# Kernel optimization log

Measured on AMD Instinct MI355X. Metric: run time of the kernel, lower is better.

## Reference

```python
import jax, jax.numpy as jnp
import numpy as np

K = 128
HEADS = 8
B = 4
T = 2048


def setup_inputs() -> dict:
    key = jax.random.key(0)
    ks = jax.random.split(key, 6)
    x = jax.random.normal(ks[0], (B, T, K), dtype=jnp.float32)
    s = 1.0 / np.sqrt(K)
    # torch nn.Linear weights are (out_features, in_features)
    Wq = jax.random.uniform(ks[1], (HEADS * K, K), dtype=jnp.float32, minval=-s, maxval=s)
    Wk = jax.random.uniform(ks[2], (HEADS * K, K), dtype=jnp.float32, minval=-s, maxval=s)
    Wv = jax.random.uniform(ks[3], (HEADS * K, K), dtype=jnp.float32, minval=-s, maxval=s)
    su = 1.0 / np.sqrt(HEADS * K)
    Wu = jax.random.uniform(ks[4], (K, HEADS * K), dtype=jnp.float32, minval=-su, maxval=su)
    bu = jax.random.uniform(ks[5], (K,), dtype=jnp.float32, minval=-su, maxval=su)
    return {"x": x, "Wq": Wq, "Wk": Wk, "Wv": Wv, "Wu": Wu, "bu": bu}


def reference(x, Wq, Wk, Wv, Wu, bu):
    b, t, k = x.shape
    h = HEADS
    # project: Linear(k, k*h) then view(b,t,h,k); weight reshaped to (h, k_out, k_in)
    q = jnp.einsum('btk,hdk->bhtd', x, Wq.reshape(h, k, k))
    kk = jnp.einsum('btk,hdk->bhtd', x, Wk.reshape(h, k, k))
    v = jnp.einsum('btk,hdk->bhtd', x, Wv.reshape(h, k, k))
    scale = jnp.asarray(k, x.dtype) ** 0.25
    q = q / scale
    kk = kk / scale
    dot = jnp.einsum('bhtd,bhsd->bhts', q, kk)  # [b,h,t,t]
    att = jax.nn.softmax(dot, axis=-1)
    out = jnp.einsum('bhts,bhsd->bhtd', att, v)  # [b,h,t,k]
    out = out.transpose(0, 2, 1, 3).reshape(b, t, h * k)
    return out @ Wu.T + bu
```

## Files before the change

### kernel.cpp

```cpp
#include <hip/hip_runtime.h>
#include <cmath>

namespace {

constexpr int HEADS = 8;
constexpr int Bn = 4;
constexpr int Tn = 2048;
constexpr int Dn = 128;
constexpr float Q_PRESCALE = 0.1275174340f;

typedef _Float16 half8 __attribute__((ext_vector_type(8)));
typedef _Float16 half4 __attribute__((ext_vector_type(4)));
typedef _Float16 half2v __attribute__((ext_vector_type(2)));
typedef float f32x4 __attribute__((ext_vector_type(4)));
typedef float f32x16 __attribute__((ext_vector_type(16)));
typedef unsigned int u32;
typedef unsigned int u32x4 __attribute__((ext_vector_type(4)));

__global__ __launch_bounds__(256) void cast_kernel(
    const float* __restrict__ x, const float* __restrict__ Wq, const float* __restrict__ Wk,
    const float* __restrict__ Wv, const float* __restrict__ Wu, _Float16* __restrict__ xh,
    _Float16* __restrict__ WH) {
  const int idx = blockIdx.x * 256 + threadIdx.x;
  const size_t base = (size_t)idx * 8;
  const float* src;
  _Float16* dst;
  if (base < 1048576) {
    src = x + base;
    dst = xh + base;
  } else {
    const size_t r = base - 1048576;
    const int s = (int)(r >> 17);
    src = ((s == 0) ? Wq : (s == 1) ? Wk : (s == 2) ? Wv : Wu) + (r & 131071);
    dst = WH + r;
  }
  const float4 a = *reinterpret_cast<const float4*>(src);
  const float4 b = *reinterpret_cast<const float4*>(src + 4);
  half8 h;
  h[0] = (_Float16)a.x; h[1] = (_Float16)a.y; h[2] = (_Float16)a.z; h[3] = (_Float16)a.w;
  h[4] = (_Float16)b.x; h[5] = (_Float16)b.y; h[6] = (_Float16)b.z; h[7] = (_Float16)b.w;
  *reinterpret_cast<half8*>(dst) = h;
}

__global__ __launch_bounds__(256, 4) void proj_kernel(const _Float16* __restrict__ xh,
                                                      const _Float16* __restrict__ WH,
                                                      _Float16* __restrict__ Qh,
                                                      _Float16* __restrict__ Kh,
                                                      _Float16* __restrict__ Vt) {
  __shared__ _Float16 sB[128 * 136];
  const int tid = threadIdx.x;
  const int w = tid >> 6, lane = tid & 63, quad = lane >> 4, l16 = lane & 15;
  const int m0 = blockIdx.x * 128;
  const int n0 = blockIdx.y * 128;

#pragma unroll
  for (int it = 0; it < 8; ++it) {
    const int fid = tid + it * 256;
    const int r = fid >> 4, g = fid & 15;
    const half8 v = *reinterpret_cast<const half8*>(WH + (size_t)(n0 + r) * 128 + g * 8);
    const int p = g ^ (r & 15);
    *reinterpret_cast<half8*>(sB + r * 128 + p * 8) = v;
  }

  half8 af[2][4];
  const _Float16* xp = xh + (size_t)(m0 + w * 32 + l16) * 128 + quad * 8;
#pragma unroll
  for (int mt = 0; mt < 2; ++mt)
#pragma unroll
    for (int kk = 0; kk < 4; ++kk)
      af[mt][kk] = *reinterpret_cast<const half8*>(xp + mt * 16 * 128 + kk * 32);

  __syncthreads();

  f32x4 acc[2][8];
#pragma unroll
  for (int mt = 0; mt < 2; ++mt)
#pragma unroll
    for (int nt = 0; nt < 8; ++nt) acc[mt][nt] = (f32x4){0.f, 0.f, 0.f, 0.f};

#pragma unroll
  for (int kk = 0; kk < 4; ++kk)
#pragma unroll
    for (int nt = 0; nt < 8; ++nt) {
      const int r = nt * 16 + l16;
      const int p = (kk * 4 + quad) ^ l16;
      const half8 bf = *reinterpret_cast<const half8*>(sB + r * 128 + p * 8);
      acc[0][nt] = __builtin_amdgcn_mfma_f32_16x16x32_f16(af[0][kk], bf, acc[0][nt], 0, 0, 0);
      acc[1][nt] = __builtin_amdgcn_mfma_f32_16x16x32_f16(af[1][kk], bf, acc[1][nt], 0, 0, 0);
    }

  const int sel = n0 >> 10;
  const int h = (n0 >> 7) & 7;
  const int b = m0 >> 11;
  const int t0b = m0 & 2047;
  const int bh = b * HEADS + h;
  const float scale = (sel == 0) ? Q_PRESCALE : 1.0f;

  __syncthreads();

  if (sel < 2) {
#pragma unroll
    for (int mt = 0; mt < 2; ++mt)
#pragma unroll
      for (int nt = 0; nt < 8; ++nt)
#pragma unroll
        for (int r = 0; r < 4; ++r)
          sB[(w * 32 + mt * 16 + quad * 4 + r) * 136 + nt * 16 + l16] =
              (_Float16)(acc[mt][nt][r] * scale);
  } else {
#pragma unroll
    for (int mt = 0; mt < 2; ++mt)
#pragma unroll
      for (int nt = 0; nt < 8; ++nt)
#pragma unroll
        for (int r = 0; r < 4; ++r)
          sB[(nt * 16 + l16) * 136 + w * 32 + mt * 16 + quad * 4 + r] = (_Float16)acc[mt][nt][r];
  }
  __syncthreads();

  _Float16* dstbase;
  size_t rstride;
  if (sel == 0) {
    dstbase = Qh + ((size_t)bh * Tn + t0b) * Dn;
    rstride = Dn;
  } else if (sel == 1) {
    dstbase = Kh + ((size_t)bh * Tn + t0b) * Dn;
    rstride = Dn;
  } else {
    dstbase = Vt + ((size_t)bh * Dn) * Tn + t0b;
    rstride = Tn;
  }
#pragma unroll
  for (int it = 0; it < 8; ++it) {
    const int fid = tid + it * 256;
    const int r = fid >> 4, g = fid & 15;
    const half8 v = *reinterpret_cast<const half8*>(sB + r * 136 + g * 8);
    *reinterpret_cast<half8*>(dstbase + (size_t)r * rstride + g * 8) = v;
  }
}

__global__ __launch_bounds__(512, 2) void flash_kernel(const _Float16* __restrict__ Qh,
                                                       const _Float16* __restrict__ Kh,
                                                       const _Float16* __restrict__ Vt,
                                                       _Float16* __restrict__ Obh) {
  __shared__ _Float16 sAll[40960];

  const int tid = threadIdx.x;
  const int w = tid >> 6;
  const int lane = tid & 63;
  const int l31 = lane & 31;
  const int h = lane >> 5;
  const int lid = blockIdx.x + 8 * blockIdx.y;
  const int xcd = lid & 7, j = lid >> 3;
  const int bh = xcd * 4 + (j >> 3);
  const int qt = j & 7;
  constexpr int NT = Tn / 64;

  half8 qf[8];
  {
    const _Float16* Qp = Qh + ((size_t)bh * Tn + qt * 256 + w * 32 + l31) * Dn + h * 8;
#pragma unroll
    for (int ds = 0; ds < 8; ++ds) qf[ds] = *reinterpret_cast<const half8*>(Qp + ds * 16);
  }

  const _Float16* Kp = Kh + (size_t)bh * Tn * Dn;
  const _Float16* Vp = Vt + (size_t)bh * Dn * Tn;

  f32x16 o[4];
#pragma unroll
  for (int db = 0; db < 4; ++db) o[db] = (f32x16)(0.f);
  float lsum = 0.f;

  half8 kreg[2], vreg[2];
  const int kr = tid >> 4, kg = tid & 15;
  const int vr = tid >> 3, vg = tid & 7;
  const int vG = (vg >> 1) * 2;
  const int vO = (vg & 1) * 4;

#pragma unroll
  for (int it = 0; it < 2; ++it) {
    kreg[it] = *reinterpret_cast<const half8*>(Kp + (size_t)(kr + it * 32) * Dn + kg * 8);
    vreg[it] = *reinterpret_cast<const half8*>(Vp + (size_t)(vr + it * 64) * Tn + vg * 8);
  }
  {
    _Float16* sK0 = sAll;
    _Float16* sV0 = sAll + 16384;
#pragma unroll
    for (int it = 0; it < 2; ++it) {
      const int r = kr + it * 32;
      const int p = kg ^ (r & 15);
      *reinterpret_cast<half8*>(sK0 + r * 128 + p * 8) = kreg[it];
      const int rv = vr + it * 64;
      const int sw = (rv & 7) ^ ((rv >> 1) & 4);
      const half8 v = vreg[it];
      half4 lo, hi;
      lo[0] = v[0]; lo[1] = v[1]; lo[2] = v[2]; lo[3] = v[3];
      hi[0] = v[4]; hi[1] = v[5]; hi[2] = v[6]; hi[3] = v[7];
      *reinterpret_cast<half4*>(sV0 + rv * 64 + ((vG ^ sw) * 8) + vO) = lo;
      *reinterpret_cast<half4*>(sV0 + rv * 64 + (((vG + 1) ^ sw) * 8) + vO) = hi;
    }
  }
#pragma unroll
  for (int it = 0; it < 2; ++it) {
    kreg[it] = *reinterpret_cast<const half8*>(Kp + (size_t)(64 + kr + it * 32) * Dn + kg * 8);
    vreg[it] = *reinterpret_cast<const half8*>(Vp + (size_t)(vr + it * 64) * Tn + 64 + vg * 8);
  }
  __syncthreads();

  f32x16 scA[2], scB[2];
  scA[0] = (f32x16)(0.f);
  scA[1] = (f32x16)(0.f);
#pragma unroll
  for (int ds = 0; ds < 8; ++ds) {
    const int p = (ds * 2 + h) ^ (l31 & 15);
    const half8 kf0 = *reinterpret_cast<const half8*>(sAll + l31 * 128 + p * 8);
    const half8 kf1 = *reinterpret_cast<const half8*>(sAll + (32 + l31) * 128 + p * 8);
    scA[0] = __builtin_amdgcn_mfma_f32_32x32x16_f16(kf0, qf[ds], scA[0], 0, 0, 0);
    scA[1] = __builtin_amdgcn_mfma_f32_32x32x16_f16(kf1, qf[ds], scA[1], 0, 0, 0);
  }

  auto step = [&](int t, f32x16 (&sc)[2], f32x16 (&sn)[2]) {
    _Float16* sKn = sAll + ((t + 1) & 1) * 8192;
    _Float16* sVc = sAll + 16384 + (t % 3) * 8192;
    _Float16* sVn = sAll + 16384 + ((t + 1) % 3) * 8192;

    if (t + 1 < NT) {
#pragma unroll
      for (int it = 0; it < 2; ++it) {
        const int r = kr + it * 32;
        const int p = kg ^ (r & 15);
        *reinterpret_cast<half8*>(sKn + r * 128 + p * 8) = kreg[it];
        const int rv = vr + it * 64;
        const int sw = (rv & 7) ^ ((rv >> 1) & 4);
        const half8 v = vreg[it];
        half4 lo, hi;
        lo[0] = v[0]; lo[1] = v[1]; lo[2] = v[2]; lo[3] = v[3];
        hi[0] = v[4]; hi[1] = v[5]; hi[2] = v[6]; hi[3] = v[7];
        *reinterpret_cast<half4*>(sVn + rv * 64 + ((vG ^ sw) * 8) + vO) = lo;
        *reinterpret_cast<half4*>(sVn + rv * 64 + (((vG + 1) ^ sw) * 8) + vO) = hi;
      }
    }
    __syncthreads();
    if (t + 2 < NT) {
      const _Float16* knext = Kp + (size_t)(t + 2) * 64 * Dn;
      const _Float16* vnext = Vp + (t + 2) * 64;
#pragma unroll
      for (int it = 0; it < 2; ++it) {
        kreg[it] = *reinterpret_cast<const half8*>(knext + (size_t)(kr + it * 32) * Dn + kg * 8);
        vreg[it] = *reinterpret_cast<const half8*>(vnext + (size_t)(vr + it * 64) * Tn + vg * 8);
      }
    }

    if (t + 1 < NT) {
      sn[0] = (f32x16)(0.f);
      sn[1] = (f32x16)(0.f);
    }

    half8 bfr[4];
#pragma unroll
    for (int i = 0; i < 2; ++i) {
      const int kb = i;
      {
        u32 pk[8];
        float part = 0.f;
#pragma unroll
        for (int j2 = 0; j2 < 8; ++j2) {
          const float e0 = __builtin_amdgcn_exp2f(sc[kb][2 * j2]);
          const float e1 = __builtin_amdgcn_exp2f(sc[kb][2 * j2 + 1]);
          part += e0 + e1;
          half2v hp = {(_Float16)e0, (_Float16)e1};
          pk[j2] = __builtin_bit_cast(u32, hp);
        }
        lsum += part;
        u32x4 beven = {pk[0], pk[1], pk[2], pk[3]};
        u32x4 bodd = {pk[4], pk[5], pk[6], pk[7]};
        bfr[kb * 2] = __builtin_bit_cast(half8, beven);
        bfr[kb * 2 + 1] = __builtin_bit_cast(half8, bodd);
      }
      if (t + 1 < NT) {
        __builtin_amdgcn_s_setprio(1);
#pragma unroll
        for (int dd = 0; dd < 4; ++dd) {
          const int ds = 4 * i + dd;
          const int p = (ds * 2 + h) ^ (l31 & 15);
          const half8 kf0 = *reinterpret_cast<const half8*>(sKn + l31 * 128 + p * 8);
          const half8 kf1 = *reinterpret_cast<const half8*>(sKn + (32 + l31) * 128 + p * 8);
          sn[0] = __builtin_amdgcn_mfma_f32_32x32x16_f16(kf0, qf[ds], sn[0], 0, 0, 0);
          sn[1] = __builtin_amdgcn_mfma_f32_32x32x16_f16(kf1, qf[ds], sn[1], 0, 0, 0);
        }
        __builtin_amdgcn_s_setprio(0);
      }
      if (i >= 1) {
        __builtin_amdgcn_s_setprio(1);
#pragma unroll
        for (int kk = 0; kk < 2; ++kk) {
          const int kb16 = kk;
#pragma unroll
          for (int db = 0; db < 4; ++db) {
            const int r = db * 32 + l31;
            const int pv = (kb16 * 2 + h) ^ ((r & 7) ^ ((r >> 1) & 4));
            const half8 vf = *reinterpret_cast<const half8*>(sVc + r * 64 + pv * 8);
            o[db] = __builtin_amdgcn_mfma_f32_32x32x16_f16(vf, bfr[kb16], o[db], 0, 0, 0);
          }
        }
        __builtin_amdgcn_s_setprio(0);
      }
    }
    __builtin_amdgcn_s_setprio(1);
#pragma unroll
    for (int kk = 2; kk < 4; ++kk) {
      const int kb16 = kk;
#pragma unroll
      for (int db = 0; db < 4; ++db) {
        const int r = db * 32 + l31;
        const int pv = (kb16 * 2 + h) ^ ((r & 7) ^ ((r >> 1) & 4));
        const half8 vf = *reinterpret_cast<const half8*>(sVc + r * 64 + pv * 8);
        o[db] = __builtin_amdgcn_mfma_f32_32x32x16_f16(vf, bfr[kb16], o[db], 0, 0, 0);
      }
    }
    __builtin_amdgcn_s_setprio(0);
  };

  for (int st = 0; st < NT; st += 2) {
    step(st, scA, scB);
    step(st + 1, scB, scA);
  }

  float inv;
  {
    float ls = lsum;
    ls += __shfl_xor(ls, 32);
    inv = 1.0f / ls;
  }

  __syncthreads();
  _Float16* const sO = sAll + w * 4096;

  {
    const int qrow = l31;
#pragma unroll
    for (int db = 0; db < 4; ++db)
#pragma unroll
      for (int grp = 0; grp < 4; ++grp) {
        const int d0 = db * 32 + grp * 8 + h * 4;
        half4 hv;
#pragma unroll
        for (int i = 0; i < 4; ++i) hv[i] = (_Float16)(o[db][grp * 4 + i] * inv);
        const int idx = qrow * 128 + (((d0 >> 3) ^ (qrow & 15)) << 3) + (d0 & 7);
        *reinterpret_cast<half4*>(sO + idx) = hv;
      }
  }
  const int b = bh >> 3, hh = bh & 7;
#pragma unroll
  for (int it = 0; it < 8; ++it) {
    const int idx = lane + it * 64;
    const int row = idx >> 4, g = idx & 15;
    const half8 v = *reinterpret_cast<const half8*>(sO + row * 128 + ((g ^ (row & 15)) << 3));
    const size_t t = (size_t)(b * Tn + qt * 256 + w * 32 + row);
    *reinterpret_cast<half8*>(Obh + t * (HEADS * Dn) + hh * 128 + g * 8) = v;
  }
}

__global__ __launch_bounds__(256, 2) void outproj_kernel(const _Float16* __restrict__ Obh,
                                                         const _Float16* __restrict__ Wuh,
                                                         const float* __restrict__ bu,
                                                         float* __restrict__ out) {
  __shared__ float sR[4 * 32 * 128];
  const int tid = threadIdx.x;
  const int w = tid >> 6, lane = tid & 63, quad = lane >> 4, l16 = lane & 15;
  const int r0 = blockIdx.x * 32;

  f32x4 acc[2][8];
#pragma unroll
  for (int mt = 0; mt < 2; ++mt)
#pragma unroll
    for (int nt = 0; nt < 8; ++nt) acc[mt][nt] = (f32x4){0.f, 0.f, 0.f, 0.f};

  const _Float16* ap = Obh + (size_t)(r0 + l16) * 1024 + w * 256 + quad * 8;
  const _Float16* bp = Wuh + (size_t)l16 * 1024 + w * 256 + quad * 8;

#pragma unroll
  for (int kk = 0; kk < 8; ++kk) {
    const half8 a0 = *reinterpret_cast<const half8*>(ap + kk * 32);
    const half8 a1 = *reinterpret_cast<const half8*>(ap + 16 * 1024 + kk * 32);
#pragma unroll
    for (int nt = 0; nt < 8; ++nt) {
      const half8 bf = *reinterpret_cast<const half8*>(bp + (size_t)nt * 16 * 1024 + kk * 32);
      acc[0][nt] = __builtin_amdgcn_mfma_f32_16x16x32_f16(a0, bf, acc[0][nt], 0, 0, 0);
      acc[1][nt] = __builtin_amdgcn_mfma_f32_16x16x32_f16(a1, bf, acc[1][nt], 0, 0, 0);
    }
  }

#pragma unroll
  for (int mt = 0; mt < 2; ++mt)
#pragma unroll
    for (int nt = 0; nt < 8; ++nt)
#pragma unroll
      for (int r = 0; r < 4; ++r)
        sR[w * 4096 + (mt * 16 + quad * 4 + r) * 128 + nt * 16 + l16] = acc[mt][nt][r];
  __syncthreads();

#pragma unroll
  for (int it = 0; it < 16; ++it) {
    const int idx = tid + it * 256;
    const int row = idx >> 7, col = idx & 127;
    const float v = sR[idx] + sR[4096 + idx] + sR[8192 + idx] + sR[12288 + idx] + bu[col];
    out[(size_t)(r0 + row) * Dn + col] = v;
  }
}

}

extern "C" void kernel_launch(void* const* d_in, const int* in_sizes, int n_in, void* d_out,
                              int out_size, void* d_ws, size_t ws_size, hipStream_t stream) {
  (void)in_sizes; (void)n_in; (void)out_size; (void)ws_size;
  const float* x = (const float*)d_in[0];
  const float* Wq = (const float*)d_in[1];
  const float* Wk = (const float*)d_in[2];
  const float* Wv = (const float*)d_in[3];
  const float* Wu = (const float*)d_in[4];
  const float* bu = (const float*)d_in[5];
  float* out = (float*)d_out;

  constexpr size_t NE = (size_t)Bn * HEADS * Tn * Dn;
  char* ws = (char*)d_ws;
  _Float16* xh = (_Float16*)ws;
  _Float16* WH = (_Float16*)(ws + 2097152);
  _Float16* Qh = (_Float16*)(ws + 4194304);
  _Float16* Kh = (_Float16*)(ws + 4194304 + NE * 2);
  _Float16* Vt = (_Float16*)(ws + 4194304 + NE * 4);
  _Float16* Obh = (_Float16*)(ws + 4194304 + NE * 6);
  _Float16* Wuh = WH + 393216;

  cast_kernel<<<dim3(768), 256, 0, stream>>>(x, Wq, Wk, Wv, Wu, xh, WH);
  proj_kernel<<<dim3(64, 24), 256, 0, stream>>>(xh, WH, Qh, Kh, Vt);
  flash_kernel<<<dim3(8, 32), 512, 0, stream>>>(Qh, Kh, Vt, Obh);
  outproj_kernel<<<dim3(256), 256, 0, stream>>>(Obh, Wuh, bu, out);
}
```

Measured before the change: 165.9 us.

## Use 128-key tiles with double-buffered LDS and drop the QK/PV software pipeline

Doubles the key/value tile from 64 to 128 rows, which halves the number of loop iterations and barriers, and grows shared memory to 128KB of double-buffered K and V. The previous schedule computed the next tile's QK scores while running the current tile's PV MMAs. That is replaced with a straightforward per-tile sequence: all QK MFMAs, then exp and PV MFMAs per 32-key block. This removes cross-iteration score registers and the triple-buffered V, but gives up the QK/PV overlap. The larger LDS footprint may also cut blocks per CU under the launch bounds of (512,2).

```diff
diff --git a/kernel.cpp b/kernel.cpp
--- a/kernel.cpp
+++ b/kernel.cpp
@@ -143,7 +143,7 @@
                                                        const _Float16* __restrict__ Kh,
                                                        const _Float16* __restrict__ Vt,
                                                        _Float16* __restrict__ Obh) {
-  __shared__ _Float16 sAll[40960];
+  __shared__ _Float16 sAll[65536];
 
   const int tid = threadIdx.x;
   const int w = tid >> 6;
@@ -154,7 +154,8 @@
   const int xcd = lid & 7, j = lid >> 3;
   const int bh = xcd * 4 + (j >> 3);
   const int qt = j & 7;
-  constexpr int NT = Tn / 64;
+  constexpr int KT = 128;
+  constexpr int NT = Tn / KT;
 
   half8 qf[8];
   {
@@ -171,159 +172,109 @@
   for (int db = 0; db < 4; ++db) o[db] = (f32x16)(0.f);
   float lsum = 0.f;
 
-  half8 kreg[2], vreg[2];
+  half8 kreg[4], vreg[4];
   const int kr = tid >> 4, kg = tid & 15;
-  const int vr = tid >> 3, vg = tid & 7;
-  const int vG = (vg >> 1) * 2;
-  const int vO = (vg & 1) * 4;
-
-#pragma unroll
-  for (int it = 0; it < 2; ++it) {
-    kreg[it] = *reinterpret_cast<const half8*>(Kp + (size_t)(kr + it * 32) * Dn + kg * 8);
-    vreg[it] = *reinterpret_cast<const half8*>(Vp + (size_t)(vr + it * 64) * Tn + vg * 8);
-  }
-  {
-    _Float16* sK0 = sAll;
-    _Float16* sV0 = sAll + 16384;
-#pragma unroll
-    for (int it = 0; it < 2; ++it) {
+  const int vd = tid >> 4, cg = tid & 15;
+  const int vG = (cg >> 1) * 2;
+  const int vO = (cg & 1) * 4;
+
+  auto stageK = [&](_Float16* sK) {
+#pragma unroll
+    for (int it = 0; it < 4; ++it) {
       const int r = kr + it * 32;
       const int p = kg ^ (r & 15);
-      *reinterpret_cast<half8*>(sK0 + r * 128 + p * 8) = kreg[it];
-      const int rv = vr + it * 64;
-      const int sw = (rv & 7) ^ ((rv >> 1) & 4);
+      *reinterpret_cast<half8*>(sK + r * 128 + p * 8) = kreg[it];
+    }
+  };
+  auto stageV = [&](_Float16* sV) {
+#pragma unroll
+    for (int it = 0; it < 4; ++it) {
+      const int d = vd + it * 32;
+      const int sw = (d & 7) ^ ((d >> 1) & 4);
       const half8 v = vreg[it];
       half4 lo, hi;
       lo[0] = v[0]; lo[1] = v[1]; lo[2] = v[2]; lo[3] = v[3];
       hi[0] = v[4]; hi[1] = v[5]; hi[2] = v[6]; hi[3] = v[7];
-      *reinterpret_cast<half4*>(sV0 + rv * 64 + ((vG ^ sw) * 8) + vO) = lo;
-      *reinterpret_cast<half4*>(sV0 + rv * 64 + (((vG + 1) ^ sw) * 8) + vO) = hi;
-    }
-  }
-#pragma unroll
-  for (int it = 0; it < 2; ++it) {
-    kreg[it] = *reinterpret_cast<const half8*>(Kp + (size_t)(64 + kr + it * 32) * Dn + kg * 8);
-    vreg[it] = *reinterpret_cast<const half8*>(Vp + (size_t)(vr + it * 64) * Tn + 64 + vg * 8);
-  }
-  __syncthreads();
-
-  f32x16 scA[2], scB[2];
-  scA[0] = (f32x16)(0.f);
-  scA[1] = (f32x16)(0.f);
-#pragma unroll
-  for (int ds = 0; ds < 8; ++ds) {
-    const int p = (ds * 2 + h) ^ (l31 & 15);
-    const half8 kf0 = *reinterpret_cast<const half8*>(sAll + l31 * 128 + p * 8);
-    const half8 kf1 = *reinterpret_cast<const half8*>(sAll + (32 + l31) * 128 + p * 8);
-    scA[0] = __builtin_amdgcn_mfma_f32_32x32x16_f16(kf0, qf[ds], scA[0], 0, 0, 0);
-    scA[1] = __builtin_amdgcn_mfma_f32_32x32x16_f16(kf1, qf[ds], scA[1], 0, 0, 0);
-  }
-
-  auto step = [&](int t, f32x16 (&sc)[2], f32x16 (&sn)[2]) {
-    _Float16* sKn = sAll + ((t + 1) & 1) * 8192;
-    _Float16* sVc = sAll + 16384 + (t % 3) * 8192;
-    _Float16* sVn = sAll + 16384 + ((t + 1) % 3) * 8192;
-
+      *reinterpret_cast<half4*>(sV + d * 128 + ((vG ^ sw) * 8) + vO) = lo;
+      *reinterpret_cast<half4*>(sV + d * 128 + (((vG | 1) ^ sw) * 8) + vO) = hi;
+    }
+  };
+  auto loadTile = [&](int tile) {
+    const _Float16* kp = Kp + (size_t)tile * KT * Dn;
+    const _Float16* vp = Vp + tile * KT;
+#pragma unroll
+    for (int it = 0; it < 4; ++it) {
+      kreg[it] = *reinterpret_cast<const half8*>(kp + (size_t)(kr + it * 32) * Dn + kg * 8);
+      vreg[it] = *reinterpret_cast<const half8*>(vp + (size_t)(vd + it * 32) * Tn + cg * 8);
+    }
+  };
+
+  loadTile(0);
+  stageK(sAll);
+  stageV(sAll + 32768);
+  loadTile(1);
+
+  for (int t = 0; t < NT; ++t) {
+    _Float16* sKc = sAll + (t & 1) * 16384;
+    _Float16* sKn = sAll + ((t + 1) & 1) * 16384;
+    _Float16* sVc = sAll + 32768 + (t & 1) * 16384;
+    _Float16* sVn = sAll + 32768 + ((t + 1) & 1) * 16384;
+
+    __syncthreads();
     if (t + 1 < NT) {
-#pragma unroll
-      for (int it = 0; it < 2; ++it) {
-        const int r = kr + it * 32;
-        const int p = kg ^ (r & 15);
-        *reinterpret_cast<half8*>(sKn + r * 128 + p * 8) = kreg[it];
-        const int rv = vr + it * 64;
-        const int sw = (rv & 7) ^ ((rv >> 1) & 4);
-        const half8 v = vreg[it];
-        half4 lo, hi;
-        lo[0] = v[0]; lo[1] = v[1]; lo[2] = v[2]; lo[3] = v[3];
-        hi[0] = v[4]; hi[1] = v[5]; hi[2] = v[6]; hi[3] = v[7];
-        *reinterpret_cast<half4*>(sVn + rv * 64 + ((vG ^ sw) * 8) + vO) = lo;
-        *reinterpret_cast<half4*>(sVn + rv * 64 + (((vG + 1) ^ sw) * 8) + vO) = hi;
+      stageK(sKn);
+      stageV(sVn);
+    }
+    if (t + 2 < NT) loadTile(t + 2);
+
+    f32x16 sacc[4];
+#pragma unroll
+    for (int kb = 0; kb < 4; ++kb) sacc[kb] = (f32x16)(0.f);
+    __builtin_amdgcn_s_setprio(1);
+#pragma unroll
+    for (int ds = 0; ds < 8; ++ds) {
+#pragma unroll
+      for (int kb = 0; kb < 4; ++kb) {
+        const int r = kb * 32 + l31;
+        const int p = (ds * 2 + h) ^ (r & 15);
+        const half8 kf = *reinterpret_cast<const half8*>(sKc + r * 128 + p * 8);
+        sacc[kb] = __builtin_amdgcn_mfma_f32_32x32x16_f16(kf, qf[ds], sacc[kb], 0, 0, 0);
       }
     }
-    __syncthreads();
-    if (t + 2 < NT) {
-      const _Float16* knext = Kp + (size_t)(t + 2) * 64 * Dn;
-      const _Float16* vnext = Vp + (t + 2) * 64;
-#pragma unroll
-      for (int it = 0; it < 2; ++it) {
-        kreg[it] = *reinterpret_cast<const half8*>(knext + (size_t)(kr + it * 32) * Dn + kg * 8);
-        vreg[it] = *reinterpret_cast<const half8*>(vnext + (size_t)(vr + it * 64) * Tn + vg * 8);
+    __builtin_amdgcn_s_setprio(0);
+
+#pragma unroll
+    for (int kb = 0; kb < 4; ++kb) {
+      u32 pk[8];
+      float part = 0.f;
+#pragma unroll
+      for (int j2 = 0; j2 < 8; ++j2) {
+        const float e0 = __builtin_amdgcn_exp2f(sacc[kb][2 * j2]);
+        const float e1 = __builtin_amdgcn_exp2f(sacc[kb][2 * j2 + 1]);
+        part += e0 + e1;
+        half2v hp = {(_Float16)e0, (_Float16)e1};
+        pk[j2] = __builtin_bit_cast(u32, hp);
       }
-    }
-
-    if (t + 1 < NT) {
-      sn[0] = (f32x16)(0.f);
-      sn[1] = (f32x16)(0.f);
-    }
-
-    half8 bfr[4];
-#pragma unroll
-    for (int i = 0; i < 2; ++i) {
-      const int kb = i;
-      {
-        u32 pk[8];
-        float part = 0.f;
-#pragma unroll
-        for (int j2 = 0; j2 < 8; ++j2) {
-          const float e0 = __builtin_amdgcn_exp2f(sc[kb][2 * j2]);
-          const float e1 = __builtin_amdgcn_exp2f(sc[kb][2 * j2 + 1]);
-          part += e0 + e1;
-          half2v hp = {(_Float16)e0, (_Float16)e1};
-          pk[j2] = __builtin_bit_cast(u32, hp);
+      lsum += part;
+      u32x4 beven = {pk[0], pk[1], pk[2], pk[3]};
+      u32x4 bodd = {pk[4], pk[5], pk[6], pk[7]};
+      const half8 bfr0 = __builtin_bit_cast(half8, beven);
+      const half8 bfr1 = __builtin_bit_cast(half8, bodd);
+      __builtin_amdgcn_s_setprio(1);
+#pragma unroll
+      for (int kk = 0; kk < 2; ++kk) {
+        const int kb16 = kb * 2 + kk;
+        const half8 bf = kk ? bfr1 : bfr0;
+#pragma unroll
+        for (int db = 0; db < 4; ++db) {
+          const int r = db * 32 + l31;
+          const int g = (kb16 * 2 + h) ^ ((r & 7) ^ ((r >> 1) & 4));
+          const half8 vf = *reinterpret_cast<const half8*>(sVc + r * 128 + g * 8);
+          o[db] = __builtin_amdgcn_mfma_f32_32x32x16_f16(vf, bf, o[db], 0, 0, 0);
         }
-        lsum += part;
-        u32x4 beven = {pk[0], pk[1], pk[2], pk[3]};
-        u32x4 bodd = {pk[4], pk[5], pk[6], pk[7]};
-        bfr[kb * 2] = __builtin_bit_cast(half8, beven);
-        bfr[kb * 2 + 1] = __builtin_bit_cast(half8, bodd);
       }
-      if (t + 1 < NT) {
-        __builtin_amdgcn_s_setprio(1);
-#pragma unroll
-        for (int dd = 0; dd < 4; ++dd) {
-          const int ds = 4 * i + dd;
-          const int p = (ds * 2 + h) ^ (l31 & 15);
-          const half8 kf0 = *reinterpret_cast<const half8*>(sKn + l31 * 128 + p * 8);
-          const half8 kf1 = *reinterpret_cast<const half8*>(sKn + (32 + l31) * 128 + p * 8);
-          sn[0] = __builtin_amdgcn_mfma_f32_32x32x16_f16(kf0, qf[ds], sn[0], 0, 0, 0);
-          sn[1] = __builtin_amdgcn_mfma_f32_32x32x16_f16(kf1, qf[ds], sn[1], 0, 0, 0);
-        }
-        __builtin_amdgcn_s_setprio(0);
-      }
-      if (i >= 1) {
-        __builtin_amdgcn_s_setprio(1);
-#pragma unroll
-        for (int kk = 0; kk < 2; ++kk) {
-          const int kb16 = kk;
-#pragma unroll
-          for (int db = 0; db < 4; ++db) {
-            const int r = db * 32 + l31;
-            const int pv = (kb16 * 2 + h) ^ ((r & 7) ^ ((r >> 1) & 4));
-            const half8 vf = *reinterpret_cast<const half8*>(sVc + r * 64 + pv * 8);
-            o[db] = __builtin_amdgcn_mfma_f32_32x32x16_f16(vf, bfr[kb16], o[db], 0, 0, 0);
-          }
-        }
-        __builtin_amdgcn_s_setprio(0);
-      }
-    }
-    __builtin_amdgcn_s_setprio(1);
-#pragma unroll
-    for (int kk = 2; kk < 4; ++kk) {
-      const int kb16 = kk;
-#pragma unroll
-      for (int db = 0; db < 4; ++db) {
-        const int r = db * 32 + l31;
-        const int pv = (kb16 * 2 + h) ^ ((r & 7) ^ ((r >> 1) & 4));
-        const half8 vf = *reinterpret_cast<const half8*>(sVc + r * 64 + pv * 8);
-        o[db] = __builtin_amdgcn_mfma_f32_32x32x16_f16(vf, bfr[kb16], o[db], 0, 0, 0);
-      }
-    }
-    __builtin_amdgcn_s_setprio(0);
-  };
-
-  for (int st = 0; st < NT; st += 2) {
-    step(st, scA, scB);
-    step(st + 1, scB, scA);
+      __builtin_amdgcn_s_setprio(0);
+    }
   }
 
   float inv;
```

Measured after the change: 187.0 us. +12.7%, slower.
